# Optimization experiments

Hardware: AMD Instinct MI355X
Metric: run time of the kernel (lower is better)

The kernel has to match this reference:

```python
import jax, jax.numpy as jnp
import numpy as np

N = 50000          # nodes
E = 800000         # edges (before self-loops)
IN = 128           # in_channels
C = 32             # hidden_channels
H = 4              # heads
SLOPE = 0.2        # PyG GATConv default negative_slope
NUM_CLASSES = 2


def setup_inputs() -> dict:
    key = jax.random.key(0)
    ks = jax.random.split(key, 20)
    s = 0.1
    inp = {
        "x": jax.random.normal(ks[0], (N, IN), jnp.float32),
        "edge_index": jax.random.randint(ks[1], (2, E), 0, N, jnp.int64),
        # conv1: IN -> H*C (concat)
        "W1": jax.random.normal(ks[2], (IN, H * C), jnp.float32) * s,
        "a1_src": jax.random.normal(ks[3], (H, C), jnp.float32) * s,
        "a1_dst": jax.random.normal(ks[4], (H, C), jnp.float32) * s,
        "b1": jnp.zeros((H * C,), jnp.float32),
        # conv2: H*C -> H*C (concat)
        "W2": jax.random.normal(ks[5], (H * C, H * C), jnp.float32) * s,
        "a2_src": jax.random.normal(ks[6], (H, C), jnp.float32) * s,
        "a2_dst": jax.random.normal(ks[7], (H, C), jnp.float32) * s,
        "b2": jnp.zeros((H * C,), jnp.float32),
        # conv3: H*C -> C (heads=1, concat=False)
        "W3": jax.random.normal(ks[8], (H * C, C), jnp.float32) * s,
        "a3_src": jax.random.normal(ks[9], (1, C), jnp.float32) * s,
        "a3_dst": jax.random.normal(ks[10], (1, C), jnp.float32) * s,
        "b3": jnp.zeros((C,), jnp.float32),
        # node classification head: C -> 2
        "Wc": jax.random.normal(ks[11], (C, NUM_CLASSES), jnp.float32) * s,
        "bc": jnp.zeros((NUM_CLASSES,), jnp.float32),
    }
    return inp


def gat_conv(x, src, dst, W, a_src, a_dst, b, heads, out_c, concat):
    """PyG-style GATConv with self-loops already appended to (src, dst)."""
    n = x.shape[0]
    h = (x @ W).reshape(n, heads, out_c)            # [N,H,C]
    al_src = jnp.sum(h * a_src, axis=-1)            # [N,H]
    al_dst = jnp.sum(h * a_dst, axis=-1)            # [N,H]
    e = al_src[src] + al_dst[dst]                   # [Et,H]
    e = jax.nn.leaky_relu(e, SLOPE)
    # numerically-stable segment softmax over edges sharing a destination
    emax = jax.ops.segment_max(e, dst, num_segments=n)   # every node has a self-loop
    e = jnp.exp(e - emax[dst])
    denom = jax.ops.segment_sum(e, dst, num_segments=n)
    alpha = e / (denom[dst] + 1e-16)                # [Et,H]
    msg = h[src] * alpha[:, :, None]                # [Et,H,C]
    out = jax.ops.segment_sum(msg, dst, num_segments=n)  # [N,H,C]
    out = out.reshape(n, heads * out_c) if concat else jnp.mean(out, axis=1)
    return out + b


def reference(x, edge_index, W1, a1_src, a1_dst, b1, W2, a2_src, a2_dst, b2,
              W3, a3_src, a3_dst, b3, Wc, bc):
    n = x.shape[0]
    loop = jnp.arange(n, dtype=edge_index.dtype)
    src = jnp.concatenate([edge_index[0], loop])
    dst = jnp.concatenate([edge_index[1], loop])
    h = jax.nn.elu(gat_conv(x, src, dst, W1, a1_src, a1_dst, b1, H, C, True))
    h = jax.nn.elu(gat_conv(h, src, dst, W2, a2_src, a2_dst, b2, H, C, True))
    h = gat_conv(h, src, dst, W3, a3_src, a3_dst, b3, 1, C, False)
    node_output = h @ Wc + bc                       # [N,2]
    link_embedding = h                              # [N,C]
    return (node_output, link_embedding)
```

## Files before the change

### kernel.cpp

```cpp
#include <hip/hip_runtime.h>
#include <math.h>

#define SLOPE 0.2f

__device__ __forceinline__ float lrelu(float x) { return x > 0.f ? x : SLOPE * x; }

__device__ __forceinline__ float bflo(unsigned int u) { return __uint_as_float(u << 16); }
__device__ __forceinline__ float bfhi(unsigned int u) { return __uint_as_float(u & 0xffff0000u); }
__device__ __forceinline__ unsigned short f2bf(float f) {
    unsigned int u = __float_as_uint(f);
    unsigned int r = u + 0x7fffu + ((u >> 16) & 1u);
    return (unsigned short)(r >> 16);
}

typedef short frag8 __attribute__((ext_vector_type(8)));
typedef float f32x4 __attribute__((ext_vector_type(4)));

__global__ __launch_bounds__(256) void wtrans_kernel(
    const float* __restrict__ W1, const float* __restrict__ W2,
    unsigned short* __restrict__ Wt1, unsigned short* __restrict__ Wt2)
{
    int idx = blockIdx.x * 256 + threadIdx.x;
    const float* W = W1;
    unsigned short* Wt = Wt1;
    int i = idx;
    if (idx >= 16384) { W = W2; Wt = Wt2; i = idx - 16384; }
    int n = i >> 7, k = i & 127;
    Wt[i] = f2bf(W[k * 128 + n]);
}

__global__ __launch_bounds__(256) void transform_mfma_kernel(
    const float* __restrict__ xin, const unsigned short* __restrict__ Wt,
    const float* __restrict__ a_src, const float* __restrict__ a_dst,
    unsigned short* __restrict__ hout, float* __restrict__ alsrc,
    float* __restrict__ aldst, int N)
{
    constexpr int MB = 64;
    constexpr int LDK = 136;
    __shared__ __align__(16) unsigned short xs[MB * LDK];
    __shared__ __align__(16) unsigned short wt[128 * LDK];

    const int node0 = blockIdx.x * MB;
    const int t = threadIdx.x;

    for (int i = t; i < MB * 32; i += 256) {
        int row = i >> 5, col4 = i & 31;
        ushort4 o;
        if (node0 + row < N) {
            float4 v = ((const float4*)(xin + (size_t)(node0 + row) * 128))[col4];
            o.x = f2bf(v.x); o.y = f2bf(v.y); o.z = f2bf(v.z); o.w = f2bf(v.w);
        } else {
            o.x = o.y = o.z = o.w = 0;
        }
        *(ushort4*)&xs[row * LDK + col4 * 4] = o;
    }
    for (int i = t; i < 2048; i += 256) {
        int n = i >> 4, k16 = i & 15;
        uint4 v = ((const uint4*)Wt)[i];
        *(uint4*)&wt[n * LDK + k16 * 8] = v;
    }
    __syncthreads();

    const int w    = t >> 6;
    const int lane = t & 63;
    const int r    = lane & 15;
    const int q    = lane >> 4;

    f32x4 acc[4][2];
#pragma unroll
    for (int mt = 0; mt < 4; ++mt)
#pragma unroll
        for (int nl = 0; nl < 2; ++nl)
            acc[mt][nl] = (f32x4){0.f, 0.f, 0.f, 0.f};

#pragma unroll
    for (int kk = 0; kk < 4; ++kk) {
        const int kof = kk * 32 + q * 8;
        frag8 b0 = *(const frag8*)&wt[(w * 32 + r) * LDK + kof];
        frag8 b1 = *(const frag8*)&wt[(w * 32 + 16 + r) * LDK + kof];
#pragma unroll
        for (int mt = 0; mt < 4; ++mt) {
            frag8 a = *(const frag8*)&xs[(mt * 16 + r) * LDK + kof];
            acc[mt][0] = __builtin_amdgcn_mfma_f32_16x16x32_bf16(a, b0, acc[mt][0], 0, 0, 0);
            acc[mt][1] = __builtin_amdgcn_mfma_f32_16x16x32_bf16(a, b1, acc[mt][1], 0, 0, 0);
        }
    }

    const float as0 = a_src[w * 32 + r],      ad0 = a_dst[w * 32 + r];
    const float as1 = a_src[w * 32 + 16 + r], ad1 = a_dst[w * 32 + 16 + r];
#pragma unroll
    for (int mt = 0; mt < 4; ++mt) {
#pragma unroll
        for (int reg = 0; reg < 4; ++reg) {
            float s = acc[mt][0][reg] * as0 + acc[mt][1][reg] * as1;
            float d = acc[mt][0][reg] * ad0 + acc[mt][1][reg] * ad1;
#pragma unroll
            for (int off = 1; off < 16; off <<= 1) {
                s += __shfl_xor(s, off);
                d += __shfl_xor(d, off);
            }
            if (r == 0) {
                int m = mt * 16 + q * 4 + reg;
                int n = node0 + m;
                if (n < N) {
                    alsrc[n * 4 + w] = s;
                    aldst[n * 4 + w] = d;
                }
            }
        }
    }

    __syncthreads();
#pragma unroll
    for (int mt = 0; mt < 4; ++mt)
#pragma unroll
        for (int nl = 0; nl < 2; ++nl)
#pragma unroll
            for (int reg = 0; reg < 4; ++reg) {
                int m = mt * 16 + q * 4 + reg;
                int n = w * 32 + nl * 16 + r;
                xs[m * LDK + n] = f2bf(acc[mt][nl][reg]);
            }
    __syncthreads();
    {
        int row = t >> 2, cbase = (t & 3) * 32;
        if (node0 + row < N) {
            uint4* dst = (uint4*)(hout + (size_t)(node0 + row) * 128 + cbase);
#pragma unroll
            for (int j = 0; j < 4; ++j)
                dst[j] = *(const uint4*)&xs[row * LDK + cbase + j * 8];
        }
    }
}

template <int COUT, int Hh, int NPT>
__global__ __launch_bounds__(256) void transform_kernel(
    const float* __restrict__ xin, const float* __restrict__ W,
    const float* __restrict__ a_src, const float* __restrict__ a_dst,
    unsigned short* __restrict__ hout, float* __restrict__ alsrc,
    float* __restrict__ aldst, int N)
{
    constexpr int JT = COUT / 4;
    constexpr int GROUPS = 256 / JT;
    constexpr int NB = GROUPS * NPT;
    constexpr int PAD = 4;
    __shared__ __align__(16) float xs[NB][128 + PAD];

    const int node0 = blockIdx.x * NB;
    const int total4 = NB * 32;
    const int lim4 = (N - node0) * 32;
    const float4* src4 = (const float4*)(xin + (size_t)node0 * 128);
    for (int i = threadIdx.x; i < total4; i += 256) {
        int row = i >> 5, col = i & 31;
        float4 v = (i < lim4) ? src4[i] : make_float4(0.f, 0.f, 0.f, 0.f);
        *(float4*)&xs[row][col << 2] = v;
    }
    __syncthreads();

    const int jt = threadIdx.x % JT;
    const int g  = threadIdx.x / JT;
    const int j4 = jt * 4;

    float4 acc[NPT];
#pragma unroll
    for (int m = 0; m < NPT; ++m) acc[m] = make_float4(0.f, 0.f, 0.f, 0.f);

    const float4* Wf4 = (const float4*)W;
    for (int k4 = 0; k4 < 32; ++k4) {
        float4 w0 = Wf4[(4 * k4 + 0) * JT + jt];
        float4 w1 = Wf4[(4 * k4 + 1) * JT + jt];
        float4 w2 = Wf4[(4 * k4 + 2) * JT + jt];
        float4 w3 = Wf4[(4 * k4 + 3) * JT + jt];
#pragma unroll
        for (int m = 0; m < NPT; ++m) {
            float4 xv = *(const float4*)&xs[g * NPT + m][k4 << 2];
            acc[m].x += xv.x * w0.x + xv.y * w1.x + xv.z * w2.x + xv.w * w3.x;
            acc[m].y += xv.x * w0.y + xv.y * w1.y + xv.z * w2.y + xv.w * w3.y;
            acc[m].z += xv.x * w0.z + xv.y * w1.z + xv.z * w2.z + xv.w * w3.z;
            acc[m].w += xv.x * w0.w + xv.y * w1.w + xv.z * w2.w + xv.w * w3.w;
        }
    }

    const float4 as4 = ((const float4*)a_src)[jt];
    const float4 ad4 = ((const float4*)a_dst)[jt];
    const int hh = j4 >> 5;

#pragma unroll
    for (int m = 0; m < NPT; ++m) {
        int n = node0 + g * NPT + m;
        float4 v = acc[m];
        float sv = v.x * as4.x + v.y * as4.y + v.z * as4.z + v.w * as4.w;
        float dv = v.x * ad4.x + v.y * ad4.y + v.z * ad4.z + v.w * ad4.w;
#pragma unroll
        for (int off = 4; off >= 1; off >>= 1) {
            sv += __shfl_xor(sv, off);
            dv += __shfl_xor(dv, off);
        }
        if (n < N) {
            ushort4 hp;
            hp.x = f2bf(v.x); hp.y = f2bf(v.y);
            hp.z = f2bf(v.z); hp.w = f2bf(v.w);
            ((ushort4*)(hout + (size_t)n * COUT))[jt] = hp;
            if ((jt & 7) == 0) {
                alsrc[n * Hh + hh] = sv;
                aldst[n * Hh + hh] = dv;
            }
        }
    }
}

#define BKT_CAP 2048
#define NBKT_MAX 1024
#define CH_BIN 4096

__global__ __launch_bounds__(1024) void bin_kernel(
    const int* __restrict__ src, const int* __restrict__ dst,
    int* __restrict__ bcnt, unsigned int* __restrict__ tmp, int E, int nbkt)
{
    __shared__ int hist[NBKT_MAX];
    __shared__ int base[NBKT_MAX];
    const int e0 = blockIdx.x * CH_BIN;
    const int e1 = min(e0 + CH_BIN, E);

    for (int b = threadIdx.x; b < nbkt; b += 1024) hist[b] = 0;
    __syncthreads();
    for (int e = e0 + threadIdx.x; e < e1; e += 1024) {
        int d = __builtin_nontemporal_load(dst + e);
        atomicAdd(&hist[d >> 6], 1);
    }
    __syncthreads();
    for (int b = threadIdx.x; b < nbkt; b += 1024) {
        int c = hist[b];
        base[b] = (c > 0) ? atomicAdd(&bcnt[b << 4], c) : 0;
        hist[b] = 0;
    }
    __syncthreads();
    for (int e = e0 + threadIdx.x; e < e1; e += 1024) {
        int d = __builtin_nontemporal_load(dst + e);
        int s = __builtin_nontemporal_load(src + e);
        int b = d >> 6;
        int pos = base[b] + atomicAdd(&hist[b], 1);
        if (pos < BKT_CAP)
            tmp[((size_t)b << 11) + pos] =
                ((unsigned int)s << 6) | (unsigned int)(d & 63);
    }
}

__global__ __launch_bounds__(256) void hist_kernel(
    const unsigned int* __restrict__ tmp, const int* __restrict__ bcnt,
    int* __restrict__ deg, int N)
{
    int b = blockIdx.x;
    __shared__ int hist[64];
    if (threadIdx.x < 64) hist[threadIdx.x] = 0;
    __syncthreads();
    int cnt = min(bcnt[b << 4], BKT_CAP);
    const unsigned int* tb = tmp + ((size_t)b << 11);
    for (int i = threadIdx.x; i < cnt; i += 256)
        atomicAdd(&hist[tb[i] & 63u], 1);
    __syncthreads();
    if (threadIdx.x < 64) {
        int node = (b << 6) + threadIdx.x;
        if (node < N) deg[node] = hist[threadIdx.x];
    }
}

__global__ __launch_bounds__(256) void block_sum_kernel(
    const int* __restrict__ deg, int* __restrict__ blocksums, int N)
{
    int base = blockIdx.x * 4096 + threadIdx.x * 16;
    int s = 0;
#pragma unroll
    for (int i = 0; i < 16; ++i) {
        int idx = base + i;
        if (idx < N) s += deg[idx];
    }
#pragma unroll
    for (int off = 1; off < 64; off <<= 1) s += __shfl_xor(s, off);
    __shared__ int wsum[4];
    if ((threadIdx.x & 63) == 0) wsum[threadIdx.x >> 6] = s;
    __syncthreads();
    if (threadIdx.x == 0)
        blocksums[blockIdx.x] = wsum[0] + wsum[1] + wsum[2] + wsum[3];
}

__global__ __launch_bounds__(64) void scan_sums_kernel(
    const int* __restrict__ blocksums, int* __restrict__ blockbase,
    int* __restrict__ total_out, int nb)
{
    int tid = threadIdx.x;
    int orig = (tid < nb) ? blocksums[tid] : 0;
    int v = orig;
#pragma unroll
    for (int off = 1; off < 64; off <<= 1) {
        int t = __shfl_up(v, off);
        if (tid >= off) v += t;
    }
    if (tid < nb) blockbase[tid] = v - orig;
    if (tid == nb - 1) *total_out = v;
}

__global__ __launch_bounds__(256) void scan_final_kernel(
    const int* __restrict__ deg, const int* __restrict__ blockbase,
    int* __restrict__ offsets, int N)
{
    int base = blockIdx.x * 4096 + threadIdx.x * 16;
    int v[16];
    int s = 0;
#pragma unroll
    for (int i = 0; i < 16; ++i) {
        int idx = base + i;
        v[i] = (idx < N) ? deg[idx] : 0;
        s += v[i];
    }
    int lane = threadIdx.x & 63, wid = threadIdx.x >> 6;
    int incl = s;
#pragma unroll
    for (int off = 1; off < 64; off <<= 1) {
        int t = __shfl_up(incl, off);
        if (lane >= off) incl += t;
    }
    __shared__ int wsum[4];
    if (lane == 63) wsum[wid] = incl;
    __syncthreads();
    int woff = 0;
    for (int i = 0; i < wid; ++i) woff += wsum[i];
    int run = blockbase[blockIdx.x] + woff + incl - s;
#pragma unroll
    for (int i = 0; i < 16; ++i) {
        int idx = base + i;
        if (idx < N) offsets[idx] = run;
        run += v[i];
    }
}

__global__ __launch_bounds__(256) void place_kernel(
    const unsigned int* __restrict__ tmp, const int* __restrict__ bcnt,
    const int* __restrict__ offsets, int* __restrict__ src_sorted, int N)
{
    int b = blockIdx.x;
    __shared__ int cur[64];
    if (threadIdx.x < 64) {
        int node = (b << 6) + threadIdx.x;
        cur[threadIdx.x] = (node < N) ? offsets[node] : 0;
    }
    __syncthreads();
    int cnt = min(bcnt[b << 4], BKT_CAP);
    const unsigned int* tb = tmp + ((size_t)b << 11);
    for (int i = threadIdx.x; i < cnt; i += 256) {
        unsigned int p = tb[i];
        int pos = atomicAdd(&cur[p & 63u], 1);
        src_sorted[pos] = (int)(p >> 6);
    }
}

__device__ __forceinline__ void fma8(const uint4& p, float w, float* a) {
    a[0] += w * bflo(p.x); a[1] += w * bfhi(p.x);
    a[2] += w * bflo(p.y); a[3] += w * bfhi(p.y);
    a[4] += w * bflo(p.z); a[5] += w * bfhi(p.z);
    a[6] += w * bflo(p.w); a[7] += w * bfhi(p.w);
}

template <int Hh, int Cc, bool DO_ELU>
__global__ __launch_bounds__(256) void gat_agg_kernel(
    const int* __restrict__ offsets, const int* __restrict__ src_sorted,
    const unsigned short* __restrict__ h, const float* __restrict__ alsrc,
    const float* __restrict__ aldst, const float* __restrict__ bias,
    float* __restrict__ outf, int N)
{
    constexpr int HC  = Hh * Cc;
    constexpr int TPN = HC / 8;
    constexpr int NPB = 256 / TPN;
    constexpr int CHUNK = 64;
    __shared__ int   s_src[NPB][CHUNK];
    __shared__ __align__(16) float s_w[NPB][CHUNK][Hh];
    __shared__ int   s_nch[NPB];

    const int g  = threadIdx.x / TPN;
    const int lt = threadIdx.x % TPN;
    const int n  = blockIdx.x * NPB + g;
    const bool valid = n < N;

    int off0 = 0, deg = 0;
    if (valid) { off0 = offsets[n]; deg = offsets[n + 1] - off0; }
    if (lt == 0) s_nch[g] = (deg + CHUNK - 1) / CHUNK;
    __syncthreads();
    int maxch = 0;
#pragma unroll
    for (int i = 0; i < NPB; ++i) maxch = max(maxch, s_nch[i]);

    const int hh = (lt * 8) / Cc;
    float adv[Hh];
    if (valid) {
        if constexpr (Hh == 4) {
            float4 t = ((const float4*)aldst)[n];
            adv[0] = t.x; adv[1] = t.y; adv[2] = t.z; adv[3] = t.w;
        } else {
            adv[0] = aldst[n];
        }
    }

    const uint4* h4 = (const uint4*)h;

    float a[8] = {0.f, 0.f, 0.f, 0.f, 0.f, 0.f, 0.f, 0.f};
    float den = 0.f;
    for (int ch = 0; ch < maxch; ++ch) {
        int base = ch * CHUNK;
        int cnt = deg - base;
        cnt = cnt < 0 ? 0 : (cnt > CHUNK ? CHUNK : cnt);
        __syncthreads();
        for (int i = lt; i < cnt; i += TPN) {
            int s = src_sorted[off0 + base + i];
            s_src[g][i] = s;
            if constexpr (Hh == 4) {
                float4 av = ((const float4*)alsrc)[s];
                ((float4*)&s_w[g][i][0])[0] = make_float4(
                    __expf(lrelu(av.x + adv[0])), __expf(lrelu(av.y + adv[1])),
                    __expf(lrelu(av.z + adv[2])), __expf(lrelu(av.w + adv[3])));
            } else {
                s_w[g][i][0] = __expf(lrelu(alsrc[s] + adv[0]));
            }
        }
        __syncthreads();
        int i = 0;
        for (; i + 1 < cnt; i += 2) {
            int s0 = s_src[g][i], s1 = s_src[g][i + 1];
            float w0 = s_w[g][i][hh], w1 = s_w[g][i + 1][hh];
            uint4 p0 = h4[(size_t)s0 * TPN + lt];
            uint4 p1 = h4[(size_t)s1 * TPN + lt];
            fma8(p0, w0, a);
            fma8(p1, w1, a);
            den += w0 + w1;
        }
        if (i < cnt) {
            int s0 = s_src[g][i];
            float w0 = s_w[g][i][hh];
            uint4 p0 = h4[(size_t)s0 * TPN + lt];
            fma8(p0, w0, a);
            den += w0;
        }
    }

    if (valid) {
        float wself = __expf(lrelu(alsrc[n * Hh + hh] + adv[hh]));
        uint4 p = h4[(size_t)n * TPN + lt];
        fma8(p, wself, a);
        den += wself + 1e-16f;
        float inv = 1.f / den;
        float4 bv0 = ((const float4*)bias)[lt * 2];
        float4 bv1 = ((const float4*)bias)[lt * 2 + 1];
        float o[8];
        o[0] = a[0] * inv + bv0.x; o[1] = a[1] * inv + bv0.y;
        o[2] = a[2] * inv + bv0.z; o[3] = a[3] * inv + bv0.w;
        o[4] = a[4] * inv + bv1.x; o[5] = a[5] * inv + bv1.y;
        o[6] = a[6] * inv + bv1.z; o[7] = a[7] * inv + bv1.w;
        if (DO_ELU) {
#pragma unroll
            for (int q = 0; q < 8; ++q)
                o[q] = o[q] > 0.f ? o[q] : __expf(o[q]) - 1.f;
        }
        float4* op = (float4*)(outf + (size_t)n * HC);
        op[lt * 2]     = make_float4(o[0], o[1], o[2], o[3]);
        op[lt * 2 + 1] = make_float4(o[4], o[5], o[6], o[7]);
    }
}

__global__ __launch_bounds__(256) void head_kernel(
    const float* __restrict__ h3, const float* __restrict__ Wc,
    const float* __restrict__ bc, float* __restrict__ out, int N)
{
    int t = blockIdx.x * 256 + threadIdx.x;
    int n = t / 2, k = t % 2;
    if (n >= N) return;
    float s = bc[k];
#pragma unroll
    for (int c = 0; c < 32; ++c) s += h3[(size_t)n * 32 + c] * Wc[c * 2 + k];
    out[(size_t)n * 2 + k] = s;
}

extern "C" void kernel_launch(void* const* d_in, const int* in_sizes, int n_in,
                              void* d_out, int out_size, void* d_ws, size_t ws_size,
                              hipStream_t stream)
{
    const float* x   = (const float*)d_in[0];
    const int*   ei  = (const int*)d_in[1];
    const float* W1  = (const float*)d_in[2];
    const float* a1s = (const float*)d_in[3];
    const float* a1d = (const float*)d_in[4];
    const float* b1  = (const float*)d_in[5];
    const float* W2  = (const float*)d_in[6];
    const float* a2s = (const float*)d_in[7];
    const float* a2d = (const float*)d_in[8];
    const float* b2  = (const float*)d_in[9];
    const float* W3  = (const float*)d_in[10];
    const float* a3s = (const float*)d_in[11];
    const float* a3d = (const float*)d_in[12];
    const float* b3  = (const float*)d_in[13];
    const float* Wc  = (const float*)d_in[14];
    const float* bc  = (const float*)d_in[15];

    const int N = in_sizes[0] / 128;
    const int E = in_sizes[1] / 2;
    const int* srcIdx = ei;
    const int* dstIdx = ei + E;

    const int NBKT = (N + 63) >> 6;

    float* ws    = (float*)d_ws;
    float* fbuf  = ws;
    float* alsrc = fbuf + (size_t)N * 128;
    float* aldst = alsrc + (size_t)N * 4;
    unsigned short* hbuf = (unsigned short*)(aldst + (size_t)N * 4);
    int* deg        = (int*)(hbuf + (size_t)N * 128);
    int* offsets    = deg + N;
    int* src_sorted = offsets + N + 1;
    int* blocksums  = src_sorted + E;
    int* blockbase  = blocksums + 64;
    uintptr_t wp = ((uintptr_t)(blockbase + 64) + 15) & ~(uintptr_t)15;
    unsigned short* wt1 = (unsigned short*)wp;
    unsigned short* wt2 = wt1 + 16384;
    int* bcnt       = (int*)(wt2 + 16384);
    unsigned int* tmp = (unsigned int*)(bcnt + (size_t)NBKT * 16);

    float* node_out = (float*)d_out;
    float* link_out = node_out + (size_t)N * 2;

    const int nb = (N + 4095) / 4096;
    const int nbBin = (E + CH_BIN - 1) / CH_BIN;

    wtrans_kernel<<<128, 256, 0, stream>>>(W1, W2, wt1, wt2);
    hipMemsetAsync(bcnt, 0, (size_t)NBKT * 16 * sizeof(int), stream);
    bin_kernel<<<nbBin, 1024, 0, stream>>>(srcIdx, dstIdx, bcnt, tmp, E, NBKT);
    hist_kernel<<<NBKT, 256, 0, stream>>>(tmp, bcnt, deg, N);
    block_sum_kernel<<<nb, 256, 0, stream>>>(deg, blocksums, N);
    scan_sums_kernel<<<1, 64, 0, stream>>>(blocksums, blockbase, offsets + N, nb);
    scan_final_kernel<<<nb, 256, 0, stream>>>(deg, blockbase, offsets, N);
    place_kernel<<<NBKT, 256, 0, stream>>>(tmp, bcnt, offsets, src_sorted, N);

    transform_mfma_kernel<<<(N + 63) / 64, 256, 0, stream>>>(
        x, wt1, a1s, a1d, hbuf, alsrc, aldst, N);
    gat_agg_kernel<4, 32, true><<<(N + 15) / 16, 256, 0, stream>>>(
        offsets, src_sorted, hbuf, alsrc, aldst, b1, fbuf, N);

    transform_mfma_kernel<<<(N + 63) / 64, 256, 0, stream>>>(
        fbuf, wt2, a2s, a2d, hbuf, alsrc, aldst, N);
    gat_agg_kernel<4, 32, true><<<(N + 15) / 16, 256, 0, stream>>>(
        offsets, src_sorted, hbuf, alsrc, aldst, b2, fbuf, N);

    transform_kernel<32, 1, 4><<<(N + 127) / 128, 256, 0, stream>>>(
        fbuf, W3, a3s, a3d, hbuf, alsrc, aldst, N);
    gat_agg_kernel<1, 32, false><<<(N + 63) / 64, 256, 0, stream>>>(
        offsets, src_sorted, hbuf, alsrc, aldst, b3, link_out, N);

    head_kernel<<<(N * 2 + 255) / 256, 256, 0, stream>>>(link_out, Wc, bc, node_out, N);
}
```

Before: 295.5 us.

## Build bucket-local CSR, store intermediate features in bf16, fuse classifier head

Replaces the global degree scan (block_sum, scan_sums, scan_final, place) with a per-bucket CSR kernel. Each 64-node bucket does a local warp scan, and offsets point into fixed-capacity bucket slots, so the agg kernel now reads degree from a separate array. Intermediate layer activations are written and read as bf16 instead of fp32, halving that traffic. The classifier head is fused into the last aggregation. This removes several kernel launches and global passes, at the cost of extra bf16 rounding and a padded src_sorted buffer.

```diff
diff --git a/kernel.cpp b/kernel.cpp
--- a/kernel.cpp
+++ b/kernel.cpp
@@ -29,8 +29,9 @@
     Wt[i] = f2bf(W[k * 128 + n]);
 }
 
+template <bool BF16IN>
 __global__ __launch_bounds__(256) void transform_mfma_kernel(
-    const float* __restrict__ xin, const unsigned short* __restrict__ Wt,
+    const void* __restrict__ xin, const unsigned short* __restrict__ Wt,
     const float* __restrict__ a_src, const float* __restrict__ a_dst,
     unsigned short* __restrict__ hout, float* __restrict__ alsrc,
     float* __restrict__ aldst, int N)
@@ -43,16 +44,28 @@
     const int node0 = blockIdx.x * MB;
     const int t = threadIdx.x;
 
-    for (int i = t; i < MB * 32; i += 256) {
-        int row = i >> 5, col4 = i & 31;
-        ushort4 o;
-        if (node0 + row < N) {
-            float4 v = ((const float4*)(xin + (size_t)(node0 + row) * 128))[col4];
-            o.x = f2bf(v.x); o.y = f2bf(v.y); o.z = f2bf(v.z); o.w = f2bf(v.w);
-        } else {
-            o.x = o.y = o.z = o.w = 0;
-        }
-        *(ushort4*)&xs[row * LDK + col4 * 4] = o;
+    if constexpr (BF16IN) {
+        const unsigned short* xb = (const unsigned short*)xin;
+        for (int i = t; i < MB * 16; i += 256) {
+            int row = i >> 4, c16 = i & 15;
+            uint4 v = make_uint4(0u, 0u, 0u, 0u);
+            if (node0 + row < N)
+                v = ((const uint4*)(xb + (size_t)(node0 + row) * 128))[c16];
+            *(uint4*)&xs[row * LDK + c16 * 8] = v;
+        }
+    } else {
+        const float* xf = (const float*)xin;
+        for (int i = t; i < MB * 32; i += 256) {
+            int row = i >> 5, col4 = i & 31;
+            ushort4 o;
+            if (node0 + row < N) {
+                float4 v = ((const float4*)(xf + (size_t)(node0 + row) * 128))[col4];
+                o.x = f2bf(v.x); o.y = f2bf(v.y); o.z = f2bf(v.z); o.w = f2bf(v.w);
+            } else {
+                o.x = o.y = o.z = o.w = 0;
+            }
+            *(ushort4*)&xs[row * LDK + col4 * 4] = o;
+        }
     }
     for (int i = t; i < 2048; i += 256) {
         int n = i >> 4, k16 = i & 15;
@@ -135,7 +148,7 @@
 
 template <int COUT, int Hh, int NPT>
 __global__ __launch_bounds__(256) void transform_kernel(
-    const float* __restrict__ xin, const float* __restrict__ W,
+    const unsigned short* __restrict__ xin, const float* __restrict__ W,
     const float* __restrict__ a_src, const float* __restrict__ a_dst,
     unsigned short* __restrict__ hout, float* __restrict__ alsrc,
     float* __restrict__ aldst, int N)
@@ -147,13 +160,16 @@
     __shared__ __align__(16) float xs[NB][128 + PAD];
 
     const int node0 = blockIdx.x * NB;
-    const int total4 = NB * 32;
-    const int lim4 = (N - node0) * 32;
-    const float4* src4 = (const float4*)(xin + (size_t)node0 * 128);
-    for (int i = threadIdx.x; i < total4; i += 256) {
-        int row = i >> 5, col = i & 31;
-        float4 v = (i < lim4) ? src4[i] : make_float4(0.f, 0.f, 0.f, 0.f);
-        *(float4*)&xs[row][col << 2] = v;
+    for (int i = threadIdx.x; i < NB * 16; i += 256) {
+        int row = i >> 4, c16 = i & 15;
+        uint4 v = make_uint4(0u, 0u, 0u, 0u);
+        if (node0 + row < N)
+            v = ((const uint4*)(xin + (size_t)(node0 + row) * 128))[c16];
+        float* xp = &xs[row][c16 * 8];
+        xp[0] = bflo(v.x); xp[1] = bfhi(v.x);
+        xp[2] = bflo(v.y); xp[3] = bfhi(v.y);
+        xp[4] = bflo(v.z); xp[5] = bfhi(v.z);
+        xp[6] = bflo(v.w); xp[7] = bfhi(v.w);
     }
     __syncthreads();
 
@@ -246,9 +262,10 @@
     }
 }
 
-__global__ __launch_bounds__(256) void hist_kernel(
+__global__ __launch_bounds__(256) void bucket_csr_kernel(
     const unsigned int* __restrict__ tmp, const int* __restrict__ bcnt,
-    int* __restrict__ deg, int N)
+    int* __restrict__ deg, int* __restrict__ offsets,
+    int* __restrict__ src_sorted, int N)
 {
     int b = blockIdx.x;
     __shared__ int hist[64];
@@ -260,97 +277,26 @@
         atomicAdd(&hist[tb[i] & 63u], 1);
     __syncthreads();
     if (threadIdx.x < 64) {
+        int v = hist[threadIdx.x];
+        int incl = v;
+#pragma unroll
+        for (int off = 1; off < 64; off <<= 1) {
+            int t2 = __shfl_up(incl, off);
+            if (threadIdx.x >= off) incl += t2;
+        }
+        int excl = incl - v;
         int node = (b << 6) + threadIdx.x;
-        if (node < N) deg[node] = hist[threadIdx.x];
-    }
-}
-
-__global__ __launch_bounds__(256) void block_sum_kernel(
-    const int* __restrict__ deg, int* __restrict__ blocksums, int N)
-{
-    int base = blockIdx.x * 4096 + threadIdx.x * 16;
-    int s = 0;
-#pragma unroll
-    for (int i = 0; i < 16; ++i) {
-        int idx = base + i;
-        if (idx < N) s += deg[idx];
-    }
-#pragma unroll
-    for (int off = 1; off < 64; off <<= 1) s += __shfl_xor(s, off);
-    __shared__ int wsum[4];
-    if ((threadIdx.x & 63) == 0) wsum[threadIdx.x >> 6] = s;
-    __syncthreads();
-    if (threadIdx.x == 0)
-        blocksums[blockIdx.x] = wsum[0] + wsum[1] + wsum[2] + wsum[3];
-}
-
-__global__ __launch_bounds__(64) void scan_sums_kernel(
-    const int* __restrict__ blocksums, int* __restrict__ blockbase,
-    int* __restrict__ total_out, int nb)
-{
-    int tid = threadIdx.x;
-    int orig = (tid < nb) ? blocksums[tid] : 0;
-    int v = orig;
-#pragma unroll
-    for (int off = 1; off < 64; off <<= 1) {
-        int t = __shfl_up(v, off);
-        if (tid >= off) v += t;
-    }
-    if (tid < nb) blockbase[tid] = v - orig;
-    if (tid == nb - 1) *total_out = v;
-}
-
-__global__ __launch_bounds__(256) void scan_final_kernel(
-    const int* __restrict__ deg, const int* __restrict__ blockbase,
-    int* __restrict__ offsets, int N)
-{
-    int base = blockIdx.x * 4096 + threadIdx.x * 16;
-    int v[16];
-    int s = 0;
-#pragma unroll
-    for (int i = 0; i < 16; ++i) {
-        int idx = base + i;
-        v[i] = (idx < N) ? deg[idx] : 0;
-        s += v[i];
-    }
-    int lane = threadIdx.x & 63, wid = threadIdx.x >> 6;
-    int incl = s;
-#pragma unroll
-    for (int off = 1; off < 64; off <<= 1) {
-        int t = __shfl_up(incl, off);
-        if (lane >= off) incl += t;
-    }
-    __shared__ int wsum[4];
-    if (lane == 63) wsum[wid] = incl;
-    __syncthreads();
-    int woff = 0;
-    for (int i = 0; i < wid; ++i) woff += wsum[i];
-    int run = blockbase[blockIdx.x] + woff + incl - s;
-#pragma unroll
-    for (int i = 0; i < 16; ++i) {
-        int idx = base + i;
-        if (idx < N) offsets[idx] = run;
-        run += v[i];
-    }
-}
-
-__global__ __launch_bounds__(256) void place_kernel(
-    const unsigned int* __restrict__ tmp, const int* __restrict__ bcnt,
-    const int* __restrict__ offsets, int* __restrict__ src_sorted, int N)
-{
-    int b = blockIdx.x;
-    __shared__ int cur[64];
-    if (threadIdx.x < 64) {
-        int node = (b << 6) + threadIdx.x;
-        cur[threadIdx.x] = (node < N) ? offsets[node] : 0;
-    }
-    __syncthreads();
-    int cnt = min(bcnt[b << 4], BKT_CAP);
-    const unsigned int* tb = tmp + ((size_t)b << 11);
+        if (node < N) {
+            deg[node] = v;
+            offsets[node] = (b << 11) + excl;
+        }
+        hist[threadIdx.x] = excl;
+    }
+    __syncthreads();
     for (int i = threadIdx.x; i < cnt; i += 256) {
         unsigned int p = tb[i];
-        int pos = atomicAdd(&cur[p & 63u], 1);
-        src_sorted[pos] = (int)(p >> 6);
+        int pos = atomicAdd(&hist[p & 63u], 1);
+        src_sorted[((size_t)b << 11) + pos] = (int)(p >> 6);
     }
 }
 
@@ -361,12 +307,14 @@
     a[6] += w * bflo(p.w); a[7] += w * bfhi(p.w);
 }
 
-template <int Hh, int Cc, bool DO_ELU>
+template <int Hh, int Cc, bool DO_ELU, bool OUTBF, bool FUSE_HEAD>
 __global__ __launch_bounds__(256) void gat_agg_kernel(
-    const int* __restrict__ offsets, const int* __restrict__ src_sorted,
+    const int* __restrict__ offsets, const int* __restrict__ deg_arr,
+    const int* __restrict__ src_sorted,
     const unsigned short* __restrict__ h, const float* __restrict__ alsrc,
     const float* __restrict__ aldst, const float* __restrict__ bias,
-    float* __restrict__ outf, int N)
+    void* __restrict__ outv, const float* __restrict__ Wc,
+    const float* __restrict__ bc, float* __restrict__ node_out, int N)
 {
     constexpr int HC  = Hh * Cc;
     constexpr int TPN = HC / 8;
@@ -382,7 +330,7 @@
     const bool valid = n < N;
 
     int off0 = 0, deg = 0;
-    if (valid) { off0 = offsets[n]; deg = offsets[n + 1] - off0; }
+    if (valid) { off0 = offsets[n]; deg = deg_arr[n]; }
     if (lt == 0) s_nch[g] = (deg + CHUNK - 1) / CHUNK;
     __syncthreads();
     int maxch = 0;
@@ -459,23 +407,36 @@
             for (int q = 0; q < 8; ++q)
                 o[q] = o[q] > 0.f ? o[q] : __expf(o[q]) - 1.f;
         }
-        float4* op = (float4*)(outf + (size_t)n * HC);
-        op[lt * 2]     = make_float4(o[0], o[1], o[2], o[3]);
-        op[lt * 2 + 1] = make_float4(o[4], o[5], o[6], o[7]);
-    }
-}
-
-__global__ __launch_bounds__(256) void head_kernel(
-    const float* __restrict__ h3, const float* __restrict__ Wc,
-    const float* __restrict__ bc, float* __restrict__ out, int N)
-{
-    int t = blockIdx.x * 256 + threadIdx.x;
-    int n = t / 2, k = t % 2;
-    if (n >= N) return;
-    float s = bc[k];
-#pragma unroll
-    for (int c = 0; c < 32; ++c) s += h3[(size_t)n * 32 + c] * Wc[c * 2 + k];
-    out[(size_t)n * 2 + k] = s;
+        if constexpr (OUTBF) {
+            unsigned short* ob = (unsigned short*)outv;
+            uint4 pk;
+            pk.x = (unsigned int)f2bf(o[0]) | ((unsigned int)f2bf(o[1]) << 16);
+            pk.y = (unsigned int)f2bf(o[2]) | ((unsigned int)f2bf(o[3]) << 16);
+            pk.z = (unsigned int)f2bf(o[4]) | ((unsigned int)f2bf(o[5]) << 16);
+            pk.w = (unsigned int)f2bf(o[6]) | ((unsigned int)f2bf(o[7]) << 16);
+            ((uint4*)(ob + (size_t)n * HC))[lt] = pk;
+        } else {
+            float* of = (float*)outv;
+            float4* op = (float4*)(of + (size_t)n * HC);
+            op[lt * 2]     = make_float4(o[0], o[1], o[2], o[3]);
+            op[lt * 2 + 1] = make_float4(o[4], o[5], o[6], o[7]);
+        }
+        if constexpr (FUSE_HEAD) {
+            float s0 = 0.f, s1 = 0.f;
+#pragma unroll
+            for (int q = 0; q < 8; ++q) {
+                int c = lt * 8 + q;
+                s0 += o[q] * Wc[c * 2];
+                s1 += o[q] * Wc[c * 2 + 1];
+            }
+            s0 += __shfl_xor(s0, 1); s0 += __shfl_xor(s0, 2);
+            s1 += __shfl_xor(s1, 1); s1 += __shfl_xor(s1, 2);
+            if (lt == 0) {
+                node_out[(size_t)n * 2]     = s0 + bc[0];
+                node_out[(size_t)n * 2 + 1] = s1 + bc[1];
+            }
+        }
+    }
 }
 
 extern "C" void kernel_launch(void* const* d_in, const int* in_sizes, int n_in,
@@ -506,51 +467,44 @@
 
     const int NBKT = (N + 63) >> 6;
 
-    float* ws    = (float*)d_ws;
-    float* fbuf  = ws;
-    float* alsrc = fbuf + (size_t)N * 128;
+    float* alsrc = (float*)d_ws;
     float* aldst = alsrc + (size_t)N * 4;
-    unsigned short* hbuf = (unsigned short*)(aldst + (size_t)N * 4);
+    unsigned short* fb16 = (unsigned short*)(aldst + (size_t)N * 4);
+    unsigned short* hbuf = fb16 + (size_t)N * 128;
     int* deg        = (int*)(hbuf + (size_t)N * 128);
     int* offsets    = deg + N;
-    int* src_sorted = offsets + N + 1;
-    int* blocksums  = src_sorted + E;
-    int* blockbase  = blocksums + 64;
-    uintptr_t wp = ((uintptr_t)(blockbase + 64) + 15) & ~(uintptr_t)15;
+    uintptr_t wp = ((uintptr_t)(offsets + N) + 15) & ~(uintptr_t)15;
     unsigned short* wt1 = (unsigned short*)wp;
     unsigned short* wt2 = wt1 + 16384;
     int* bcnt       = (int*)(wt2 + 16384);
-    unsigned int* tmp = (unsigned int*)(bcnt + (size_t)NBKT * 16);
+    int* src_sorted = bcnt + (size_t)NBKT * 16;
+    unsigned int* tmp = (unsigned int*)(src_sorted + (size_t)NBKT * BKT_CAP);
 
     float* node_out = (float*)d_out;
     float* link_out = node_out + (size_t)N * 2;
 
-    const int nb = (N + 4095) / 4096;
     const int nbBin = (E + CH_BIN - 1) / CH_BIN;
 
     wtrans_kernel<<<128, 256, 0, stream>>>(W1, W2, wt1, wt2);
     hipMemsetAsync(bcnt, 0, (size_t)NBKT * 16 * sizeof(int), stream);
     bin_kernel<<<nbBin, 1024, 0, stream>>>(srcIdx, dstIdx, bcnt, tmp, E, NBKT);
-    hist_kernel<<<NBKT, 256, 0, stream>>>(tmp, bcnt, deg, N);
-    block_sum_kernel<<<nb, 256, 0, stream>>>(deg, blocksums, N);
-    scan_sums_kernel<<<1, 64, 0, stream>>>(blocksums, blockbase, offsets + N, nb);
-    scan_final_kernel<<<nb, 256, 0, stream>>>(deg, blockbase, offsets, N);
-    place_kernel<<<NBKT, 256, 0, stream>>>(tmp, bcnt, offsets, src_sorted, N);
-
-    transform_mfma_kernel<<<(N + 63) / 64, 256, 0, stream>>>(
+    bucket_csr_kernel<<<NBKT, 256, 0, stream>>>(tmp, bcnt, deg, offsets, src_sorted, N);
+
+    transform_mfma_kernel<false><<<(N + 63) / 64, 256, 0, stream>>>(
         x, wt1, a1s, a1d, hbuf, alsrc, aldst, N);
-    gat_agg_kernel<4, 32, true><<<(N + 15) / 16, 256, 0, stream>>>(
-        offsets, src_sorted, hbuf, alsrc, aldst, b1, fbuf, N);
-
-    transform_mfma_kernel<<<(N + 63) / 64, 256, 0, stream>>>(
-        fbuf, wt2, a2s, a2d, hbuf, alsrc, aldst, N);
-    gat_agg_kernel<4, 32, true><<<(N + 15) / 16, 256, 0, stream>>>(
-        offsets, src_sorted, hbuf, alsrc, aldst, b2, fbuf, N);
+    gat_agg_kernel<4, 32, true, true, false><<<(N + 15) / 16, 256, 0, stream>>>(
+        offsets, deg, src_sorted, hbuf, alsrc, aldst, b1, fb16,
+        nullptr, nullptr, nullptr, N);
+
+    transform_mfma_kernel<true><<<(N + 63) / 64, 256, 0, stream>>>(
+        fb16, wt2, a2s, a2d, hbuf, alsrc, aldst, N);
+    gat_agg_kernel<4, 32, true, true, false><<<(N + 15) / 16, 256, 0, stream>>>(
+        offsets, deg, src_sorted, hbuf, alsrc, aldst, b2, fb16,
+        nullptr, nullptr, nullptr, N);
 
     transform_kernel<32, 1, 4><<<(N + 127) / 128, 256, 0, stream>>>(
-        fbuf, W3, a3s, a3d, hbuf, alsrc, aldst, N);
-    gat_agg_kernel<1, 32, false><<<(N + 63) / 64, 256, 0, stream>>>(
-        offsets, src_sorted, hbuf, alsrc, aldst, b3, link_out, N);
-
-    head_kernel<<<(N * 2 + 255) / 256, 256, 0, stream>>>(link_out, Wc, bc, node_out, N);
-}
+        fb16, W3, a3s, a3d, hbuf, alsrc, aldst, N);
+    gat_agg_kernel<1, 32, false, false, true><<<(N + 63) / 64, 256, 0, stream>>>(
+        offsets, deg, src_sorted, hbuf, alsrc, aldst, b3, link_out,
+        Wc, bc, node_out, N);
+}
```

After: 272.7 us. 7.7% less time.
